# Performance work log

Hardware: AMD Instinct MI355X
Metric: run time of the kernel (lower is better)

## Reference

```python
import jax, jax.numpy as jnp
import numpy as np

B, P, PD = 32, 196, 768          # batch, n_subdivs, subdiv feature dim
D, H, L, NC = 768, 12, 8, 1000   # n_dims, n_heads, n_blocks, n_classes
HD = D // H                      # per-head dim (64)


def _pos_emb(n_pos, d):
    # faithful to _sinusoidal_positional_embeddings: row i (timestep) parity picks sin/cos
    i = jnp.arange(n_pos, dtype=jnp.float32)[:, None]
    j = jnp.arange(d, dtype=jnp.float32)[None, :]
    sin_v = jnp.sin(i / jnp.power(10000.0, j / d))
    cos_v = jnp.cos(i / jnp.power(10000.0, (j - 1.0) / d))
    return jnp.where((jnp.arange(n_pos)[:, None] % 2) == 0, sin_v, cos_v)  # (n_pos, d)


def _layernorm(x, g, b, eps=1e-5):
    m = jnp.mean(x, axis=-1, keepdims=True)
    v = jnp.var(x, axis=-1, keepdims=True)
    return (x - m) * jax.lax.rsqrt(v + eps) * g + b


def setup_inputs() -> dict:
    key = jax.random.key(0)
    ks = iter(jax.random.split(key, 16))
    nrm = lambda shape, s=0.02: jax.random.normal(next(ks), shape, jnp.float32) * s
    return {
        "x": jax.random.normal(next(ks), (B, P, PD), jnp.float32),
        "W_emb": nrm((PD, D)), "b_emb": jnp.zeros((D,), jnp.float32),
        "v_class": jax.random.uniform(next(ks), (1, D), jnp.float32),
        "ln1_g": jnp.ones((L, D), jnp.float32), "ln1_b": jnp.zeros((L, D), jnp.float32),
        "Wq": nrm((L, H, HD, HD)), "bq": jnp.zeros((L, H, HD), jnp.float32),
        "Wk": nrm((L, H, HD, HD)), "bk": jnp.zeros((L, H, HD), jnp.float32),
        "Wv": nrm((L, H, HD, HD)), "bv": jnp.zeros((L, H, HD), jnp.float32),
        "ln2_g": jnp.ones((L, D), jnp.float32), "ln2_b": jnp.zeros((L, D), jnp.float32),
        "W1": nrm((L, D, 4 * D)), "b1": jnp.zeros((L, 4 * D), jnp.float32),
        "W2": nrm((L, 4 * D, D)), "b2": jnp.zeros((L, D), jnp.float32),
        "W_cls": nrm((D, NC)), "b_cls": jnp.zeros((NC,), jnp.float32),
    }


def reference(x, W_emb, b_emb, v_class, ln1_g, ln1_b, Wq, bq, Wk, bk, Wv, bv,
              ln2_g, ln2_b, W1, b1, W2, b2, W_cls, b_cls):
    b = x.shape[0]
    pos = _pos_emb(P, D)                                  # (P, D), same for every sample
    h = x @ W_emb + b_emb + pos                           # (B, P, D)
    cls_tok = jnp.broadcast_to(v_class[None], (b, 1, D))
    h = jnp.concatenate([cls_tok, h], axis=1)             # (B, S, D), S = P + 1
    S = P + 1
    attns = []
    for l in range(L):
        # --- MHSA: each head reads only its own hd-slice of the input ---
        xn = _layernorm(h, ln1_g[l], ln1_b[l])
        xh = xn.reshape(b, S, H, HD)
        q = jnp.einsum('bshi,hij->bshj', xh, Wq[l]) + bq[l]
        k = jnp.einsum('bshi,hij->bshj', xh, Wk[l]) + bk[l]
        v = jnp.einsum('bshi,hij->bshj', xh, Wv[l]) + bv[l]
        scores = jnp.einsum('bqhj,bkhj->bhqk', q, k) / (HD ** 0.5)
        a = jax.nn.softmax(scores, axis=-1)               # (B, H, S, S)
        attns.append(jnp.mean(a, axis=1))                 # mean over heads, (B, S, S)
        o = jnp.einsum('bhqk,bkhj->bqhj', a, v).reshape(b, S, D)
        h = o + h                                         # residual 1
        # --- MLP ---
        xn2 = _layernorm(h, ln2_g[l], ln2_b[l])
        m = jax.nn.gelu(xn2 @ W1[l] + b1[l], approximate=False)
        h = m @ W2[l] + b2[l] + h                         # residual 2
    cls = h[:, 0]
    pred = jax.nn.softmax(cls @ W_cls + b_cls, axis=-1)   # (B, NC)
    return pred, jnp.stack(attns)                         # attns: (L, B, S, S)
```

## Files before the change

### kernel.cpp

```cpp
#include <hip/hip_runtime.h>
#include <cstdint>

typedef unsigned short u16;
typedef __attribute__((ext_vector_type(8))) short bf16x8;
typedef __attribute__((ext_vector_type(4))) float f32x4;

#define DEV static __device__ __forceinline__

#define BB 32
#define PP 196
#define DD 768
#define HH 12
#define HDD 64
#define SS 197
#define NTOK 6304
#define NTOKX 6272
#define NCLS 1000
#define DD4 3072
#define KPAD 224
#define NBH 384
#define NLAY 8

DEV u16 f2bf(float f){ unsigned u=__float_as_uint(f); u += 0x7FFFu + ((u>>16)&1u); return (u16)(u>>16); }
DEV float bf2f(u16 u){ return __uint_as_float(((unsigned)u)<<16); }

typedef __attribute__((address_space(1))) void gas1;
typedef __attribute__((address_space(3))) void las3;

DEV void gld16(const void* g, void* l){
  __builtin_amdgcn_global_load_lds((gas1*)(uintptr_t)g, (las3*)(unsigned)(uintptr_t)l, 16, 0, 0);
}

struct __align__(8) u16x4 { u16 x,y,z,w; };


__global__ void pos_kernel(float* __restrict__ pos){
  int idx = blockIdx.x*256 + threadIdx.x;
  if (idx >= PP*DD) return;
  int p = idx / DD, j = idx - p*DD;
  int odd = p & 1;
  float e = ((float)j - (float)odd) * (1.0f/(float)DD);
  float arg = (float)p / powf(10000.0f, e);
  pos[idx] = odd ? cosf(arg) : sinf(arg);
}

__global__ void f32_to_bf16_kernel(const float* __restrict__ in, u16* __restrict__ out, int n4){
  int i = blockIdx.x*256 + threadIdx.x;
  if (i >= n4) return;
  float4 v = reinterpret_cast<const float4*>(in)[i];
  u16x4 o = { f2bf(v.x), f2bf(v.y), f2bf(v.z), f2bf(v.w) };
  reinterpret_cast<u16x4*>(out)[i] = o;
}

__global__ void clstok_kernel(const float* __restrict__ vcls, float* __restrict__ h){
  int b = blockIdx.x;
  for (int i = threadIdx.x; i < DD; i += 256)
    h[(size_t)b*SS*DD + i] = vcls[i];
}

__global__ void transpose_kernel(const float* __restrict__ in, u16* __restrict__ out, int R, int C){
  __shared__ float tile[32][33];
  int bx = blockIdx.x*32, by = blockIdx.y*32;
  size_t zoff = (size_t)blockIdx.z * R * C;
  const float* src = in + zoff;
  u16* dst = out + zoff;
  int tx = threadIdx.x, ty = threadIdx.y;
  #pragma unroll
  for (int q=0;q<4;q++)
    tile[ty + q*8][tx] = src[(size_t)(by + ty + q*8)*C + bx + tx];
  __syncthreads();
  #pragma unroll
  for (int q=0;q<4;q++)
    dst[(size_t)(bx + ty + q*8)*R + by + tx] = f2bf(tile[tx][ty + q*8]);
}

__global__ void ln_kernel(const float* __restrict__ h, const float* __restrict__ g,
                          const float* __restrict__ b, u16* __restrict__ xn){
  int t = blockIdx.x*4 + (threadIdx.x>>6);
  int lane = threadIdx.x & 63;
  const float4* src = reinterpret_cast<const float4*>(h + (size_t)t*DD);
  float4 xv[3];
  float s = 0.f, s2 = 0.f;
  #pragma unroll
  for (int p=0;p<3;p++){
    xv[p] = src[p*64 + lane];
    s  += xv[p].x + xv[p].y + xv[p].z + xv[p].w;
    s2 += xv[p].x*xv[p].x + xv[p].y*xv[p].y + xv[p].z*xv[p].z + xv[p].w*xv[p].w;
  }
  #pragma unroll
  for (int o=32;o>0;o>>=1){ s += __shfl_xor(s,o); s2 += __shfl_xor(s2,o); }
  float mean = s * (1.f/(float)DD);
  float rstd = rsqrtf(s2*(1.f/(float)DD) - mean*mean + 1e-5f);
  #pragma unroll
  for (int p=0;p<3;p++){
    int base = p*256 + lane*4;
    u16x4 o4 = { f2bf((xv[p].x-mean)*rstd*g[base+0]+b[base+0]),
                 f2bf((xv[p].y-mean)*rstd*g[base+1]+b[base+1]),
                 f2bf((xv[p].z-mean)*rstd*g[base+2]+b[base+2]),
                 f2bf((xv[p].w-mean)*rstd*g[base+3]+b[base+3]) };
    *reinterpret_cast<u16x4*>(&xn[(size_t)t*DD + base]) = o4;
  }
}

template<int EPI>
__global__ __launch_bounds__(256) void gemm_bf16(
    const u16* __restrict__ A, const u16* __restrict__ BT, int M, int K,
    int nbm, int nbn,
    const float* __restrict__ bias, const float* __restrict__ pos,
    float* __restrict__ Hout, u16* __restrict__ Bout)
{
  __shared__ __align__(16) u16 As[2][128*32];
  __shared__ __align__(16) u16 Bs[2][128*32];
  const int tid = threadIdx.x;
  const int wave = tid>>6, lane = tid&63;

  const int nwg = nbm*nbn;
  const int wg = blockIdx.x;
  const int xcd = wg & 7, ii = wg >> 3;
  const int q8 = nwg >> 3, r8 = nwg & 7;
  const int lin = (xcd < r8 ? xcd*(q8+1) : r8*(q8+1) + (xcd-r8)*q8) + ii;
  const int bm = lin / nbn, bn = lin - bm*nbn;

  const int wr = wave>>1, wc = wave&1;

  f32x4 acc[4][4] = {};

  const int lr = lane>>2;
  const int lc = ((lane&3) ^ ((lane>>3)&3)) * 8;
  int ar0 = bm*128 + (wave*2+0)*16 + lr; if (ar0 > M-1) ar0 = M-1;
  int ar1 = bm*128 + (wave*2+1)*16 + lr; if (ar1 > M-1) ar1 = M-1;
  const u16* aS0 = A + (size_t)ar0*K + lc;
  const u16* aS1 = A + (size_t)ar1*K + lc;
  const u16* bS0 = BT + (size_t)(bn*128 + (wave*2+0)*16 + lr)*K + lc;
  const u16* bS1 = BT + (size_t)(bn*128 + (wave*2+1)*16 + lr)*K + lc;
  const int d0 = (wave*2+0)*512;
  const int d1 = (wave*2+1)*512;

  auto stage = [&](int buf, int kt){
    gld16(aS0 + kt, &As[buf][d0]);
    gld16(aS1 + kt, &As[buf][d1]);
    gld16(bS0 + kt, &Bs[buf][d0]);
    gld16(bS1 + kt, &Bs[buf][d1]);
  };
  const int rchunk = ((lane>>4) ^ (((lane&15)>>1)&3)) * 8;
  auto compute = [&](int buf){
    bf16x8 af[4], bfv[4];
    #pragma unroll
    for (int i=0;i<4;i++)
      af[i] = *reinterpret_cast<const bf16x8*>(&As[buf][(wr*64 + i*16 + (lane&15))*32 + rchunk]);
    #pragma unroll
    for (int j=0;j<4;j++)
      bfv[j] = *reinterpret_cast<const bf16x8*>(&Bs[buf][(wc*64 + j*16 + (lane&15))*32 + rchunk]);
    #pragma unroll
    for (int i=0;i<4;i++)
      #pragma unroll
      for (int j=0;j<4;j++)
        acc[i][j] = __builtin_amdgcn_mfma_f32_16x16x32_bf16(af[i], bfv[j], acc[i][j], 0, 0, 0);
  };

  const int NT = K >> 5;
  stage(0, 0);
  int cur = 0;
  for (int t = 0; t < NT; ++t){
    if (t+1 < NT){
      stage(cur^1, (t+1)*32);
      asm volatile("s_waitcnt vmcnt(4)" ::: "memory");
    } else {
      asm volatile("s_waitcnt vmcnt(0)" ::: "memory");
    }
    __builtin_amdgcn_s_barrier();
    __builtin_amdgcn_sched_barrier(0);
    compute(cur);
    __builtin_amdgcn_s_barrier();
    cur ^= 1;
  }

  const int rowb = bm*128 + wr*64 + (lane>>4)*4;
  const int colb = bn*128 + wc*64 + (lane&15);
  const int Nst = nbn * 128;
  #pragma unroll
  for (int i=0;i<4;i++){
    #pragma unroll
    for (int j=0;j<4;j++){
      int col = colb + j*16;
      #pragma unroll
      for (int r=0;r<4;r++){
        int row = rowb + i*16 + r;
        if (row >= M) continue;
        float v = acc[i][j][r];
        if (EPI == 0){
          int bb = row / PP, p = row - bb*PP;
          Hout[((size_t)(bb*SS + 1 + p))*DD + col] = v + bias[col] + pos[p*DD + col];
        } else if (EPI == 1){
          float xg = v + bias[col];
          Bout[(size_t)row*Nst + col] = f2bf(0.5f*xg*(1.f + erff(xg*0.7071067811865475f)));
        } else {
          Hout[(size_t)row*DD + col] += v + bias[col];
        }
      }
    }
  }
}

__global__ __launch_bounds__(256) void qkv_kernel(
    const u16* __restrict__ xn,
    const u16* __restrict__ WqT, const u16* __restrict__ WkT, const u16* __restrict__ WvT,
    const float* __restrict__ bq, const float* __restrict__ bk, const float* __restrict__ bv,
    u16* __restrict__ qb, u16* __restrict__ kb, u16* __restrict__ vb)
{
  const int LDA = 72;
  __shared__ __align__(16) u16 Asm[128*72];
  __shared__ __align__(16) u16 Wsm[3][64*72];
  const int tid = threadIdx.x, wave = tid>>6, lane = tid&63;
  const int bm = blockIdx.x, hd = blockIdx.y;

  #pragma unroll
  for (int ps=0; ps<4; ++ps){
    int e = (ps*256 + tid)*8;
    int row = e>>6, col = e&63;
    int gr = bm*128 + row; if (gr > NTOK-1) gr = NTOK-1;
    *reinterpret_cast<int4*>(&Asm[row*LDA + col]) =
        *reinterpret_cast<const int4*>(&xn[(size_t)gr*DD + hd*HDD + col]);
  }
  const u16* wsrc[3] = { WqT + hd*4096, WkT + hd*4096, WvT + hd*4096 };
  #pragma unroll
  for (int w=0; w<3; ++w)
    #pragma unroll
    for (int ps=0; ps<2; ++ps){
      int e = (ps*256 + tid)*8;
      int row = e>>6, col = e&63;
      *reinterpret_cast<int4*>(&Wsm[w][row*LDA + col]) =
          *reinterpret_cast<const int4*>(&wsrc[w][row*64 + col]);
    }
  __syncthreads();

  bf16x8 af[2][2];
  #pragma unroll
  for (int i=0;i<2;i++)
    #pragma unroll
    for (int kk=0;kk<2;kk++)
      af[i][kk] = *reinterpret_cast<const bf16x8*>(&Asm[(wave*32 + i*16 + (lane&15))*LDA + kk*32 + (lane>>4)*8]);

  f32x4 acc[3][2][4] = {};
  #pragma unroll
  for (int w=0;w<3;w++)
    #pragma unroll
    for (int kk=0;kk<2;kk++)
      #pragma unroll
      for (int j=0;j<4;j++){
        bf16x8 bfv = *reinterpret_cast<const bf16x8*>(&Wsm[w][(j*16 + (lane&15))*LDA + kk*32 + (lane>>4)*8]);
        #pragma unroll
        for (int i=0;i<2;i++)
          acc[w][i][j] = __builtin_amdgcn_mfma_f32_16x16x32_bf16(af[i][kk], bfv, acc[w][i][j], 0,0,0);
      }

  const float* bqh = bq + hd*HDD;
  const float* bkh = bk + hd*HDD;
  const float* bvh = bv + hd*HDD;
  #pragma unroll
  for (int i=0;i<2;i++)
    #pragma unroll
    for (int j=0;j<4;j++){
      int d = j*16 + (lane&15);
      #pragma unroll
      for (int r=0;r<4;r++){
        int t = bm*128 + wave*32 + i*16 + (lane>>4)*4 + r;
        if (t >= NTOK) continue;
        int b = t / SS, sx = t - b*SS;
        size_t bh = (size_t)b*HH + hd;
        qb[(bh*SS + sx)*HDD + d] = f2bf(acc[0][i][j][r] + bqh[d]);
        kb[(bh*SS + sx)*HDD + d] = f2bf(acc[1][i][j][r] + bkh[d]);
        vb[(bh*KPAD + sx)*HDD + d] = f2bf(acc[2][i][j][r] + bvh[d]);
      }
    }
}

__global__ __launch_bounds__(256) void attn_scores_softmax_kernel(
    const u16* __restrict__ qb, const u16* __restrict__ kb, u16* __restrict__ attn)
{
  const int LDA = 72;
  __shared__ __align__(16) u16 Qs[128*72];
  __shared__ __align__(16) u16 Ks[KPAD*72];
  const int tid = threadIdx.x, wave = tid>>6, lane = tid&63;
  const int bm = blockIdx.x, bh = blockIdx.y;

  #pragma unroll
  for (int ps=0; ps<4; ++ps){
    int e = (ps*256 + tid)*8;
    int row = e>>6, col = e&63;
    int qr = bm*128 + row; if (qr > SS-1) qr = SS-1;
    *reinterpret_cast<int4*>(&Qs[row*LDA + col]) =
        *reinterpret_cast<const int4*>(&qb[((size_t)bh*SS + qr)*HDD + col]);
  }
  #pragma unroll
  for (int ps=0; ps<7; ++ps){
    int e = (ps*256 + tid)*8;
    int row = e>>6, col = e&63;
    int kr = row; if (kr > SS-1) kr = SS-1;
    *reinterpret_cast<int4*>(&Ks[row*LDA + col]) =
        *reinterpret_cast<const int4*>(&kb[((size_t)bh*SS + kr)*HDD + col]);
  }
  __syncthreads();

  bf16x8 af[2][2];
  #pragma unroll
  for (int i=0;i<2;i++)
    #pragma unroll
    for (int kk=0;kk<2;kk++)
      af[i][kk] = *reinterpret_cast<const bf16x8*>(&Qs[(wave*32 + i*16 + (lane&15))*LDA + kk*32 + (lane>>4)*8]);

  f32x4 acc[2][14];
  #pragma unroll
  for (int i=0;i<2;i++)
    #pragma unroll
    for (int j=0;j<14;j++)
      acc[i][j] = f32x4{0.f,0.f,0.f,0.f};

  #pragma unroll
  for (int kk=0;kk<2;kk++)
    #pragma unroll
    for (int j=0;j<14;j++){
      bf16x8 bfv = *reinterpret_cast<const bf16x8*>(&Ks[(j*16 + (lane&15))*LDA + kk*32 + (lane>>4)*8]);
      #pragma unroll
      for (int i=0;i<2;i++)
        acc[i][j] = __builtin_amdgcn_mfma_f32_16x16x32_bf16(af[i][kk], bfv, acc[i][j], 0,0,0);
    }

  const int kcol = lane & 15;
  #pragma unroll
  for (int i=0;i<2;i++){
    #pragma unroll
    for (int r=0;r<4;r++){
      int qg = bm*128 + wave*32 + i*16 + (lane>>4)*4 + r;
      float vals[14];
      float mx = -1e30f;
      #pragma unroll
      for (int j=0;j<14;j++){
        int kg = j*16 + kcol;
        float v = (kg < SS) ? acc[i][j][r]*0.125f : -1e30f;
        vals[j] = v;
        mx = fmaxf(mx, v);
      }
      mx = fmaxf(mx, __shfl_xor(mx,1)); mx = fmaxf(mx, __shfl_xor(mx,2));
      mx = fmaxf(mx, __shfl_xor(mx,4)); mx = fmaxf(mx, __shfl_xor(mx,8));
      float s = 0.f;
      #pragma unroll
      for (int j=0;j<14;j++){
        int kg = j*16 + kcol;
        float e = (kg < SS) ? expf(vals[j]-mx) : 0.f;
        vals[j] = e; s += e;
      }
      s += __shfl_xor(s,1); s += __shfl_xor(s,2);
      s += __shfl_xor(s,4); s += __shfl_xor(s,8);
      float inv = 1.f / s;
      if (qg < SS){
        u16* dst = attn + ((size_t)bh*SS + qg)*KPAD;
        #pragma unroll
        for (int j=0;j<14;j++)
          dst[j*16 + kcol] = f2bf(vals[j]*inv);
      }
    }
  }
}

__global__ void attnmean_kernel(const u16* __restrict__ attn, float* __restrict__ outp){
  int qi = blockIdx.x, b = blockIdx.y, kk = threadIdx.x;
  if (kk >= SS) return;
  float s = 0.f;
  #pragma unroll
  for (int h=0; h<HH; ++h)
    s += bf2f(attn[(((size_t)b*HH + h)*SS + qi)*KPAD + kk]);
  outp[((size_t)b*SS + qi)*SS + kk] = s * (1.f/12.f);
}

__global__ __launch_bounds__(256) void av_kernel(
    const u16* __restrict__ attn, const u16* __restrict__ vb, float* __restrict__ h)
{
  const int LDA = 40;
  const int LDB = 40;
  __shared__ __align__(16) u16 Asm[128*40];
  __shared__ __align__(16) u16 Bsm[64*40];
  const int tid = threadIdx.x, wave = tid>>6, lane = tid&63;
  const int bm = blockIdx.x, bh = blockIdx.y;
  const int b = bh / HH, hd = bh - b*HH;
  f32x4 acc[2][4] = {};
  for (int k0 = 0; k0 < KPAD; k0 += 32){
    if (k0) __syncthreads();
    #pragma unroll
    for (int ps=0; ps<2; ++ps){
      int e = (ps*256 + tid)*8;
      int row = e>>5, col = e&31;
      int ar = bm*128 + row; if (ar > SS-1) ar = SS-1;
      *reinterpret_cast<int4*>(&Asm[row*LDA + col]) =
          *reinterpret_cast<const int4*>(&attn[((size_t)bh*SS + ar)*KPAD + k0 + col]);
    }
    {
      int kk = tid>>3;
      int d0 = (tid&7)*8;
      bf16x8 vv = *reinterpret_cast<const bf16x8*>(&vb[((size_t)bh*KPAD + k0 + kk)*HDD + d0]);
      #pragma unroll
      for (int q=0;q<8;q++) Bsm[(d0+q)*LDB + kk] = (u16)vv[q];
    }
    __syncthreads();
    bf16x8 af[2], bfv[4];
    #pragma unroll
    for (int i=0;i<2;i++) af[i] = *reinterpret_cast<const bf16x8*>(&Asm[(wave*32 + i*16 + (lane&15))*LDA + (lane>>4)*8]);
    #pragma unroll
    for (int j=0;j<4;j++) bfv[j] = *reinterpret_cast<const bf16x8*>(&Bsm[(j*16 + (lane&15))*LDB + (lane>>4)*8]);
    #pragma unroll
    for (int i=0;i<2;i++)
      #pragma unroll
      for (int j=0;j<4;j++)
        acc[i][j] = __builtin_amdgcn_mfma_f32_16x16x32_bf16(af[i], bfv[j], acc[i][j], 0,0,0);
  }
  #pragma unroll
  for (int i=0;i<2;i++)
    #pragma unroll
    for (int j=0;j<4;j++){
      int d = j*16 + (lane&15);
      #pragma unroll
      for (int r=0;r<4;r++){
        int sx = bm*128 + wave*32 + i*16 + (lane>>4)*4 + r;
        if (sx < SS)
          h[((size_t)b*SS + sx)*DD + hd*HDD + d] += acc[i][j][r];
      }
    }
}

__global__ __launch_bounds__(256) void logits_kernel(
    const float* __restrict__ h, const float* __restrict__ Wc,
    const float* __restrict__ bc, float* __restrict__ logits)
{
  __shared__ float xs[DD];
  const int b = blockIdx.x, tid = threadIdx.x;
  for (int i = tid; i < DD; i += 256) xs[i] = h[(size_t)b*SS*DD + i];
  __syncthreads();
  const int c = blockIdx.y*250 + tid;
  if (tid >= 250 || c >= NCLS) return;
  float acc = bc[c];
  const float* wcol = Wc + c;
  #pragma unroll 16
  for (int k = 0; k < DD; ++k)
    acc += xs[k] * wcol[(size_t)k*NCLS];
  logits[(size_t)b*NCLS + c] = acc;
}

__global__ __launch_bounds__(256) void pred_softmax_kernel(
    const float* __restrict__ logits, float* __restrict__ outp)
{
  __shared__ float red[256];
  const int b = blockIdx.x, tid = threadIdx.x;
  float acc[4], mx = -1e30f;
  #pragma unroll
  for (int m=0;m<4;m++){
    int c = tid + m*256;
    acc[m] = (c < NCLS) ? logits[(size_t)b*NCLS + c] : -1e30f;
    mx = fmaxf(mx, acc[m]);
  }
  red[tid] = mx; __syncthreads();
  for (int o=128;o>0;o>>=1){ if (tid<o) red[tid] = fmaxf(red[tid], red[tid+o]); __syncthreads(); }
  mx = red[0]; __syncthreads();
  float ex[4]; float s = 0.f;
  #pragma unroll
  for (int m=0;m<4;m++){
    int c = tid + m*256;
    ex[m] = (c < NCLS) ? expf(acc[m]-mx) : 0.f;
    s += ex[m];
  }
  red[tid] = s; __syncthreads();
  for (int o=128;o>0;o>>=1){ if (tid<o) red[tid] += red[tid+o]; __syncthreads(); }
  float inv = 1.f / red[0];
  #pragma unroll
  for (int m=0;m<4;m++){
    int c = tid + m*256;
    if (c < NCLS) outp[(size_t)b*NCLS + c] = ex[m]*inv;
  }
}

extern "C" void kernel_launch(void* const* d_in, const int* in_sizes, int n_in,
                              void* d_out, int out_size, void* d_ws, size_t ws_size,
                              hipStream_t stream)
{
  const float* x      = (const float*)d_in[0];
  const float* W_emb  = (const float*)d_in[1];
  const float* b_emb  = (const float*)d_in[2];
  const float* v_class= (const float*)d_in[3];
  const float* ln1_g  = (const float*)d_in[4];
  const float* ln1_b  = (const float*)d_in[5];
  const float* Wq     = (const float*)d_in[6];
  const float* bq     = (const float*)d_in[7];
  const float* Wk     = (const float*)d_in[8];
  const float* bk     = (const float*)d_in[9];
  const float* Wv     = (const float*)d_in[10];
  const float* bv     = (const float*)d_in[11];
  const float* ln2_g  = (const float*)d_in[12];
  const float* ln2_b  = (const float*)d_in[13];
  const float* W1     = (const float*)d_in[14];
  const float* b1     = (const float*)d_in[15];
  const float* W2     = (const float*)d_in[16];
  const float* b2     = (const float*)d_in[17];
  const float* W_cls  = (const float*)d_in[18];
  const float* b_cls  = (const float*)d_in[19];
  (void)in_sizes; (void)n_in; (void)out_size;
  float* outp = (float*)d_out;

  char* ws = (char*)d_ws;
  size_t off = 0;
  auto alloc = [&](size_t bytes)->char*{
    char* p = ws + off;
    off = (off + bytes + 255) & ~((size_t)255);
    return p;
  };
  float* pos    = (float*)alloc((size_t)PP*DD*4);
  float* hbuf   = (float*)alloc((size_t)NTOK*DD*4);
  u16*   xnb    = (u16*)  alloc((size_t)NTOK*DD*2);
  u16*   WembT  = (u16*)  alloc((size_t)DD*DD*2);
  u16*   W1Tall = (u16*)  alloc((size_t)NLAY*DD*DD4*2);
  u16*   W2Tall = (u16*)  alloc((size_t)NLAY*DD*DD4*2);
  u16*   WqT    = (u16*)  alloc((size_t)NLAY*HH*HDD*HDD*2);
  u16*   WkT    = (u16*)  alloc((size_t)NLAY*HH*HDD*HDD*2);
  u16*   WvT    = (u16*)  alloc((size_t)NLAY*HH*HDD*HDD*2);
  char*  blob   = alloc((size_t)NTOK*DD4*2);
  float* logitsb= (float*)alloc((size_t)BB*NCLS*4);
  u16* qbuf = (u16*)blob;
  u16* kbuf = qbuf + (size_t)NBH*SS*HDD;
  u16* vbuf = kbuf + (size_t)NBH*SS*HDD;
  u16* scb  = vbuf + (size_t)NBH*KPAD*HDD;
  u16* mbuf = (u16*)blob;
  u16* xbf  = scb;
  if (ws_size < off) return;

  hipMemsetAsync(vbuf, 0, (size_t)NBH*KPAD*HDD*2, stream);
  pos_kernel<<<(PP*DD+255)/256, 256, 0, stream>>>(pos);
  f32_to_bf16_kernel<<<(NTOKX*DD/4+255)/256, 256, 0, stream>>>(x, xbf, NTOKX*DD/4);
  dim3 tb(32,8);
  transpose_kernel<<<dim3(DD/32, DD/32, 1), tb, 0, stream>>>(W_emb, WembT, DD, DD);
  transpose_kernel<<<dim3(2,2,NLAY*HH), tb, 0, stream>>>(Wq, WqT, HDD, HDD);
  transpose_kernel<<<dim3(2,2,NLAY*HH), tb, 0, stream>>>(Wk, WkT, HDD, HDD);
  transpose_kernel<<<dim3(2,2,NLAY*HH), tb, 0, stream>>>(Wv, WvT, HDD, HDD);
  transpose_kernel<<<dim3(DD4/32, DD/32, NLAY), tb, 0, stream>>>(W1, W1Tall, DD, DD4);
  transpose_kernel<<<dim3(DD/32, DD4/32, NLAY), tb, 0, stream>>>(W2, W2Tall, DD4, DD);

  gemm_bf16<0><<<49*6, 256, 0, stream>>>(xbf, WembT, NTOKX, DD, 49, 6, b_emb, pos, hbuf, nullptr);
  clstok_kernel<<<BB, 256, 0, stream>>>(v_class, hbuf);

  for (int l=0; l<NLAY; ++l){
    ln_kernel<<<NTOK/4, 256, 0, stream>>>(hbuf, ln1_g + l*DD, ln1_b + l*DD, xnb);
    qkv_kernel<<<dim3(50, HH), 256, 0, stream>>>(xnb,
        WqT + (size_t)l*HH*4096, WkT + (size_t)l*HH*4096, WvT + (size_t)l*HH*4096,
        bq + l*HH*HDD, bk + l*HH*HDD, bv + l*HH*HDD, qbuf, kbuf, vbuf);
    attn_scores_softmax_kernel<<<dim3(2, NBH), 256, 0, stream>>>(qbuf, kbuf, scb);
    attnmean_kernel<<<dim3(SS, BB), 256, 0, stream>>>(scb, outp + 32000 + (size_t)l*BB*SS*SS);
    av_kernel<<<dim3(2, NBH), 256, 0, stream>>>(scb, vbuf, hbuf);
    ln_kernel<<<NTOK/4, 256, 0, stream>>>(hbuf, ln2_g + l*DD, ln2_b + l*DD, xnb);
    gemm_bf16<1><<<50*24, 256, 0, stream>>>(xnb, W1Tall + (size_t)l*DD*DD4, NTOK, DD, 50, 24,
                                            b1 + l*DD4, nullptr, nullptr, mbuf);
    gemm_bf16<2><<<50*6, 256, 0, stream>>>(mbuf, W2Tall + (size_t)l*DD*DD4, NTOK, DD4, 50, 6,
                                           b2 + l*DD, nullptr, hbuf, nullptr);
  }
  logits_kernel<<<dim3(BB, 4), 256, 0, stream>>>(hbuf, W_cls, b_cls, logitsb);
  pred_softmax_kernel<<<BB, 256, 0, stream>>>(logitsb, outp);
}
```

Before: 1.855 ms.

## Double GEMM K-tile to 64 with XOR-swizzled LDS and fast erf GELU

The bf16 GEMM's K tile grows from 32 to 64, so each double-buffered stage loads twice the data. The LDS layout uses an 8-chunk XOR swizzle, and compute runs two MFMA k-substeps per barrier pair. This halves the number of loop iterations and barriers. The exact erff in the GELU epilogue is replaced by an Abramowitz-Stegun polynomial with a hardware reciprocal and fast exp, which adds small approximation error (about 1e-7 absolute) and doubles LDS use, which may lower occupancy.

```diff
diff --git a/kernel.cpp b/kernel.cpp
--- a/kernel.cpp
+++ b/kernel.cpp
@@ -24,6 +24,17 @@
 DEV u16 f2bf(float f){ unsigned u=__float_as_uint(f); u += 0x7FFFu + ((u>>16)&1u); return (u16)(u>>16); }
 DEV float bf2f(u16 u){ return __uint_as_float(((unsigned)u)<<16); }
 
+DEV float gelu_f(float x){
+  float z  = 0.70710678118654752f * x;
+  float az = fabsf(z);
+  float t  = __builtin_amdgcn_rcpf(fmaf(0.3275911f, az, 1.f));
+  float poly = t*(0.254829592f + t*(-0.284496736f + t*(1.421413741f + t*(-1.453152027f + t*1.061405429f))));
+  float e  = __expf(-az*az);
+  float erf_abs = 1.f - poly*e;
+  float erfv = copysignf(erf_abs, x);
+  return 0.5f * x * (1.f + erfv);
+}
+
 typedef __attribute__((address_space(1))) void gas1;
 typedef __attribute__((address_space(3))) void las3;
 
@@ -109,8 +120,8 @@
     const float* __restrict__ bias, const float* __restrict__ pos,
     float* __restrict__ Hout, u16* __restrict__ Bout)
 {
-  __shared__ __align__(16) u16 As[2][128*32];
-  __shared__ __align__(16) u16 Bs[2][128*32];
+  __shared__ __align__(16) u16 As[2][128*64];
+  __shared__ __align__(16) u16 Bs[2][128*64];
   const int tid = threadIdx.x;
   const int wave = tid>>6, lane = tid&63;
 
@@ -125,46 +136,53 @@
 
   f32x4 acc[4][4] = {};
 
-  const int lr = lane>>2;
-  const int lc = ((lane&3) ^ ((lane>>3)&3)) * 8;
-  int ar0 = bm*128 + (wave*2+0)*16 + lr; if (ar0 > M-1) ar0 = M-1;
-  int ar1 = bm*128 + (wave*2+1)*16 + lr; if (ar1 > M-1) ar1 = M-1;
-  const u16* aS0 = A + (size_t)ar0*K + lc;
-  const u16* aS1 = A + (size_t)ar1*K + lc;
-  const u16* bS0 = BT + (size_t)(bn*128 + (wave*2+0)*16 + lr)*K + lc;
-  const u16* bS1 = BT + (size_t)(bn*128 + (wave*2+1)*16 + lr)*K + lc;
-  const int d0 = (wave*2+0)*512;
-  const int d1 = (wave*2+1)*512;
+  const int srow  = lane>>3;
+  const int scol  = ((lane&7) ^ srow) * 8;
+  const u16* aS[4]; const u16* bS[4];
+  #pragma unroll
+  for (int g=0; g<4; ++g){
+    int arw = bm*128 + wave*32 + g*8 + srow; if (arw > M-1) arw = M-1;
+    aS[g] = A  + (size_t)arw*K + scol;
+    bS[g] = BT + (size_t)(bn*128 + wave*32 + g*8 + srow)*K + scol;
+  }
 
   auto stage = [&](int buf, int kt){
-    gld16(aS0 + kt, &As[buf][d0]);
-    gld16(aS1 + kt, &As[buf][d1]);
-    gld16(bS0 + kt, &Bs[buf][d0]);
-    gld16(bS1 + kt, &Bs[buf][d1]);
+    #pragma unroll
+    for (int g=0; g<4; ++g){
+      gld16(aS[g] + kt, &As[buf][(wave*32 + g*8)*64]);
+      gld16(bS[g] + kt, &Bs[buf][(wave*32 + g*8)*64]);
+    }
   };
-  const int rchunk = ((lane>>4) ^ (((lane&15)>>1)&3)) * 8;
+  const int r15 = lane&15;
   auto compute = [&](int buf){
-    bf16x8 af[4], bfv[4];
-    #pragma unroll
-    for (int i=0;i<4;i++)
-      af[i] = *reinterpret_cast<const bf16x8*>(&As[buf][(wr*64 + i*16 + (lane&15))*32 + rchunk]);
-    #pragma unroll
-    for (int j=0;j<4;j++)
-      bfv[j] = *reinterpret_cast<const bf16x8*>(&Bs[buf][(wc*64 + j*16 + (lane&15))*32 + rchunk]);
-    #pragma unroll
-    for (int i=0;i<4;i++)
-      #pragma unroll
-      for (int j=0;j<4;j++)
-        acc[i][j] = __builtin_amdgcn_mfma_f32_16x16x32_bf16(af[i], bfv[j], acc[i][j], 0, 0, 0);
+    #pragma unroll
+    for (int kk=0; kk<2; ++kk){
+      bf16x8 af[4], bfv[4];
+      #pragma unroll
+      for (int i=0;i<4;i++){
+        int row = wr*64 + i*16 + r15;
+        af[i] = *reinterpret_cast<const bf16x8*>(&As[buf][row*64 + ((((lane>>4)+kk*4) ^ (lane&7))<<3)]);
+      }
+      #pragma unroll
+      for (int j=0;j<4;j++){
+        int row = wc*64 + j*16 + r15;
+        bfv[j] = *reinterpret_cast<const bf16x8*>(&Bs[buf][row*64 + ((((lane>>4)+kk*4) ^ (lane&7))<<3)]);
+      }
+      #pragma unroll
+      for (int i=0;i<4;i++)
+        #pragma unroll
+        for (int j=0;j<4;j++)
+          acc[i][j] = __builtin_amdgcn_mfma_f32_16x16x32_bf16(af[i], bfv[j], acc[i][j], 0, 0, 0);
+    }
   };
 
-  const int NT = K >> 5;
+  const int NT = K >> 6;
   stage(0, 0);
   int cur = 0;
   for (int t = 0; t < NT; ++t){
     if (t+1 < NT){
-      stage(cur^1, (t+1)*32);
-      asm volatile("s_waitcnt vmcnt(4)" ::: "memory");
+      stage(cur^1, (t+1)*64);
+      asm volatile("s_waitcnt vmcnt(8)" ::: "memory");
     } else {
       asm volatile("s_waitcnt vmcnt(0)" ::: "memory");
     }
@@ -192,8 +210,7 @@
           int bb = row / PP, p = row - bb*PP;
           Hout[((size_t)(bb*SS + 1 + p))*DD + col] = v + bias[col] + pos[p*DD + col];
         } else if (EPI == 1){
-          float xg = v + bias[col];
-          Bout[(size_t)row*Nst + col] = f2bf(0.5f*xg*(1.f + erff(xg*0.7071067811865475f)));
+          Bout[(size_t)row*Nst + col] = f2bf(gelu_f(v + bias[col]));
         } else {
           Hout[(size_t)row*DD + col] += v + bias[col];
         }
```

Result: no change. 1.878 ms (+1.3%).
